# Optimization experiments

Hardware: AMD Instinct MI355X
Metric: run time of the kernel (lower is better)

## Reference

```python
import jax, jax.numpy as jnp
import numpy as np

N_E = 4096
E_DIM = 256
BETA = 0.25


def setup_inputs() -> dict:
    key = jax.random.key(0)
    k1, k2 = jax.random.split(key)
    z = jax.random.normal(k1, (2, E_DIM, 8, 32, 32), dtype=jnp.float32)
    # torch: embedding.weight.data.uniform_(-1/n_e, 1/n_e)
    embedding_weight = jax.random.uniform(
        k2, (N_E, E_DIM), dtype=jnp.float32, minval=-1.0 / N_E, maxval=1.0 / N_E)
    ema_embedding = jnp.zeros((N_E, E_DIM), dtype=jnp.float32)
    return {"z": z, "embedding_weight": embedding_weight, "ema_embedding": ema_embedding}


def reference(z, embedding_weight, ema_embedding):
    sg = jax.lax.stop_gradient
    # [B, C, D, H, W] -> [B, D, H, W, C]
    zp = jnp.transpose(z, (0, 2, 3, 4, 1))
    zf = zp.reshape(-1, E_DIM)  # [N, e_dim]
    # pairwise squared distances: ||z||^2 + ||e||^2 - 2 z e^T  -> [N, n_e]
    d = (jnp.sum(zf * zf, axis=1, keepdims=True)
         + jnp.sum(embedding_weight * embedding_weight, axis=1)
         - 2.0 * jnp.matmul(zf, embedding_weight.T))
    min_encoding_indices = jnp.argmin(d, axis=1)  # [N]
    min_encodings = jax.nn.one_hot(min_encoding_indices, N_E, dtype=zf.dtype)  # [N, n_e]
    # one_hot @ W == gather of codebook rows
    z_q = embedding_weight[min_encoding_indices].reshape(zp.shape)
    loss = (jnp.mean((sg(z_q) - zp) ** 2)
            + BETA * jnp.mean((z_q - sg(zp)) ** 2))
    # straight-through estimator
    z_q_st = zp + sg(z_q - zp)
    # EMA buffer update (torch does this under no_grad)
    ema_new = BETA * ema_embedding + (1.0 - BETA) * sg(embedding_weight)
    e_mean = jnp.mean(min_encodings, axis=0)
    perplexity = jnp.exp(-jnp.sum(e_mean * jnp.log(e_mean + 1e-10)))
    z_q_out = jnp.transpose(z_q_st, (0, 4, 1, 2, 3))
    z_out = jnp.transpose(zp, (0, 4, 1, 2, 3))
    return (loss, z_q_out, perplexity, min_encodings,
            min_encoding_indices[:, None], z_out, ema_new)
```

## Files before the change

kernel.cpp:

```cpp
#include <hip/hip_runtime.h>
#include <math.h>


#define N_E    4096
#define EDIM   256
#define SPAT   8192
#define NROWS  16384
#define ZELEMS 4194304
#define NCHUNK 32
#define NLOSSPARTS 16384

#define OFF_LOSS    0
#define OFF_ZQ      1
#define OFF_PERP    4194305
#define OFF_ONEHOT  4194306
#define OFF_IDX     71303170
#define OFF_ZOUT    71319554
#define OFF_EMA     75513858

#define SCR_WH_F   4
#define SCR_BD2_F  524292
#define SCR_ZH_F   71319556
#define SCR_WL_F   73416708
#define SCR_BD_F   73940996
#define SCR_BI_F   74465284

#define MARG 1.5e-4f
#define GAPM 1.5e-4f

typedef unsigned short u16;
typedef short short8 __attribute__((ext_vector_type(8)));
typedef float f32x4 __attribute__((ext_vector_type(4)));
typedef const void __attribute__((address_space(1)))* gas1;
typedef void __attribute__((address_space(3)))* las3;
#define GLOAD16(g, l) __builtin_amdgcn_global_load_lds((gas1)(g), (las3)(l), 16, 0, 0)

__device__ __forceinline__ u16 f2bf(float f) {
    unsigned u = __float_as_uint(f);
    return (u16)((u + 0x7fffu + ((u >> 16) & 1u)) >> 16);
}
__device__ __forceinline__ float bf2f(u16 h) {
    return __uint_as_float(((unsigned)h) << 16);
}

__global__ __launch_bounds__(256) void se_kernel(const float* __restrict__ W,
                                                 float* __restrict__ se) {
    int wid  = (blockIdx.x * 256 + threadIdx.x) >> 6;
    int lane = threadIdx.x & 63;
    if (wid < N_E) {
        const float4 v = *(const float4*)(W + (size_t)wid * EDIM + lane * 4);
        float s = v.x * v.x + v.y * v.y + v.z * v.z + v.w * v.w;
        #pragma unroll
        for (int off = 32; off > 0; off >>= 1) s += __shfl_down(s, off);
        if (lane == 0) se[wid] = s;
    }
}

__global__ __launch_bounds__(512) void rnorm_kernel(const float* __restrict__ z,
                                                    float* __restrict__ sz) {
    const int r0 = blockIdx.x * 128;
    const int bb = r0 >> 13;
    const int sp0 = r0 & (SPAT - 1);
    const float* zb = z + (size_t)bb * (EDIM * SPAT) + sp0;
    __shared__ float szp[4][128];
    const int lr = threadIdx.x & 127, kq = threadIdx.x >> 7;
    float s = 0.f;
    const float* p = zb + lr + (size_t)(kq * 64) * SPAT;
    for (int k = 0; k < 64; ++k) {
        float v = p[(size_t)k * SPAT];
        s += v * v;
    }
    szp[kq][lr] = s;
    __syncthreads();
    if (threadIdx.x < 128)
        sz[r0 + threadIdx.x] =
            ((szp[0][threadIdx.x] + szp[1][threadIdx.x]) + szp[2][threadIdx.x]) + szp[3][threadIdx.x];
}

__global__ __launch_bounds__(256) void split_w_kernel(const float* __restrict__ W,
                                                      u16* __restrict__ wh,
                                                      u16* __restrict__ wl) {
    const size_t t = (size_t)blockIdx.x * 256 + threadIdx.x;
    const float4 v = *(const float4*)(W + t * 4);
    u16 h0 = f2bf(v.x), h1 = f2bf(v.y), h2 = f2bf(v.z), h3 = f2bf(v.w);
    u16 l0 = f2bf(v.x - bf2f(h0)), l1 = f2bf(v.y - bf2f(h1));
    u16 l2 = f2bf(v.z - bf2f(h2)), l3 = f2bf(v.w - bf2f(h3));
    uint2 hp, lp;
    hp.x = (unsigned)h0 | ((unsigned)h1 << 16); hp.y = (unsigned)h2 | ((unsigned)h3 << 16);
    lp.x = (unsigned)l0 | ((unsigned)l1 << 16); lp.y = (unsigned)l2 | ((unsigned)l3 << 16);
    *(uint2*)(wh + t * 4) = hp;
    *(uint2*)(wl + t * 4) = lp;
}

__global__ __launch_bounds__(256) void split_z_kernel(const float* __restrict__ z,
                                                      u16* __restrict__ zh) {
    __shared__ float t[128][65];
    const int tid = threadIdx.x, wid = tid >> 6, lane = tid & 63;
    const int sp0 = blockIdx.x * 64, c0 = blockIdx.y * 128, b = blockIdx.z;
    const float* zb = z + (size_t)b * (EDIM * SPAT);
    #pragma unroll
    for (int it = 0; it < 32; ++it) {
        const int cl = wid + 4 * it;
        t[cl][lane] = zb[(size_t)(c0 + cl) * SPAT + sp0 + lane];
    }
    __syncthreads();
    #pragma unroll
    for (int it = 0; it < 16; ++it) {
        const int r = wid + 4 * it;
        const float v0 = t[2 * lane][r], v1 = t[2 * lane + 1][r];
        const u16 h0 = f2bf(v0), h1 = f2bf(v1);
        const size_t row = (size_t)b * SPAT + sp0 + r;
        ((unsigned*)zh)[row * 128 + (c0 >> 1) + lane] = (unsigned)h0 | ((unsigned)h1 << 16);
    }
}

__global__ __launch_bounds__(256, 3) void argmin_kernel(
        const u16* __restrict__ zh,
        const u16* __restrict__ wh, const u16* __restrict__ wl,
        const float* __restrict__ se, const float* __restrict__ sz,
        float* __restrict__ bD, int* __restrict__ bI,
        float* __restrict__ bD2, float* __restrict__ out_onehot) {
    __shared__ u16 sW[128][64];
    __shared__ u16 sZ[128][32];
    __shared__ float mD[2][128];
    __shared__ int   mI[2][128];
    __shared__ float mD2[2][128];

    const int tid = threadIdx.x;
    const int wid = tid >> 6, lane = tid & 63;
    const int wm = wid >> 1, wn = wid & 1;
    const int lq = lane >> 4, lr = lane & 15;
    const int chunk = blockIdx.x;
    const int rbase = blockIdx.y * 128;
    const int cbase = chunk * 128;

    const u16* gw[4];
    #pragma unroll
    for (int i = 0; i < 4; ++i) {
        const int o = i * 256 + tid;
        const int row = o >> 3, g = o & 7, u = g ^ (row & 7);
        const int ks = (u & 3) * 8;
        gw[i] = (u < 4 ? wh : wl) + (size_t)(cbase + row) * EDIM + ks;
    }
    const u16* gz[2];
    #pragma unroll
    for (int j = 0; j < 2; ++j) {
        const int o = j * 256 + tid;
        const int row = o >> 2, g = o & 3, u = g ^ ((row >> 1) & 3);
        gz[j] = zh + (size_t)(rbase + row) * EDIM + u * 8;
    }

    int aoff[4][2], boff[4];
    #pragma unroll
    for (int tt = 0; tt < 4; ++tt) {
        const int cl = wn * 64 + tt * 16 + lr;
        const int s0 = lq ^ (cl & 7);
        aoff[tt][0] = cl * 128 + s0 * 16;
        aoff[tt][1] = cl * 128 + (s0 ^ 4) * 16;
        const int rl = wm * 64 + tt * 16 + lr;
        boff[tt] = rl * 64 + (lq ^ ((rl >> 1) & 3)) * 16;
    }

    f32x4 acc[4][4];
    #pragma unroll
    for (int ci = 0; ci < 4; ++ci)
        #pragma unroll
        for (int rj = 0; rj < 4; ++rj) {
            f32x4 zzz = {0.f, 0.f, 0.f, 0.f};
            acc[ci][rj] = zzz;
        }

    const char* sWb = (const char*)&sW[0][0];
    const char* sZb = (const char*)&sZ[0][0];

    for (int k0 = 0; k0 < 8; ++k0) {
        __syncthreads();
        #pragma unroll
        for (int i = 0; i < 4; ++i) {
            GLOAD16(gw[i], (char*)&sW[0][0] + (i * 256 + wid * 64) * 16);
            gw[i] += 32;
        }
        #pragma unroll
        for (int j = 0; j < 2; ++j) {
            GLOAD16(gz[j], (char*)&sZ[0][0] + (j * 256 + wid * 64) * 16);
            gz[j] += 32;
        }
        __syncthreads();

        short8 zb[4];
        #pragma unroll
        for (int rj = 0; rj < 4; ++rj)
            zb[rj] = *(const short8*)(sZb + boff[rj]);
        #pragma unroll
        for (int ci = 0; ci < 4; ++ci) {
            const short8 wah = *(const short8*)(sWb + aoff[ci][0]);
            const short8 wal = *(const short8*)(sWb + aoff[ci][1]);
            #pragma unroll
            for (int rj = 0; rj < 4; ++rj) {
                acc[ci][rj] = __builtin_amdgcn_mfma_f32_16x16x32_bf16(wah, zb[rj], acc[ci][rj], 0, 0, 0);
                acc[ci][rj] = __builtin_amdgcn_mfma_f32_16x16x32_bf16(wal, zb[rj], acc[ci][rj], 0, 0, 0);
            }
        }
    }

    f32x4 sev[4];
    #pragma unroll
    for (int ci = 0; ci < 4; ++ci)
        sev[ci] = *(const f32x4*)(se + cbase + wn * 64 + ci * 16 + lq * 4);

    #pragma unroll
    for (int rj = 0; rj < 4; ++rj) {
        const int rloc = wm * 64 + rj * 16 + lr;
        const float szr = sz[rbase + rloc];
        float b1 = 3.4e38f, b2 = 3.4e38f; int bi1 = 0x7fffffff;
        #pragma unroll
        for (int ci = 0; ci < 4; ++ci) {
            #pragma unroll
            for (int r = 0; r < 4; ++r) {
                const float q = (szr + sev[ci][r]) - 2.0f * acc[ci][rj][r];
                const int code = cbase + wn * 64 + ci * 16 + lq * 4 + r;
                if (q < b1 || (q == b1 && code < bi1)) {
                    b2 = b1; b1 = q; bi1 = code;
                } else if (q < b2) {
                    b2 = q;
                }
            }
        }
        #pragma unroll
        for (int mask = 16; mask <= 32; mask <<= 1) {
            const float od1 = __shfl_xor(b1, mask);
            const int   oi1 = __shfl_xor(bi1, mask);
            const float od2 = __shfl_xor(b2, mask);
            const bool ot = (od1 < b1) || (od1 == b1 && oi1 < bi1);
            if (ot) { b2 = fminf(b1, od2); b1 = od1; bi1 = oi1; }
            else    { b2 = fminf(b2, od1); }
        }
        if (lq == 0) {
            mD[wn][rloc]  = b1;
            mI[wn][rloc]  = bi1;
            mD2[wn][rloc] = b2;
        }
    }
    __syncthreads();
    if (tid < 128) {
        const float d0 = mD[0][tid], d1 = mD[1][tid];
        const int   i0 = mI[0][tid], i1 = mI[1][tid];
        const float s0 = mD2[0][tid], s1 = mD2[1][tid];
        float dm, sm; int im;
        if (d1 < d0 || (d1 == d0 && i1 < i0)) { dm = d1; im = i1; sm = fminf(s1, d0); }
        else                                  { dm = d0; im = i0; sm = fminf(s0, d1); }
        bD [(size_t)chunk * NROWS + rbase + tid] = dm;
        bI [(size_t)chunk * NROWS + rbase + tid] = im;
        bD2[(size_t)chunk * NROWS + rbase + tid] = sm;
    }

    {
        const int slice = blockIdx.y * 32 + blockIdx.x;
        float* oh = out_onehot + (size_t)slice * 16384;
        const float4 z4 = {0.f, 0.f, 0.f, 0.f};
        #pragma unroll
        for (int it = 0; it < 16; ++it)
            *(float4*)(oh + it * 1024 + tid * 4) = z4;
    }
}

__global__ __launch_bounds__(256) void resolve_kernel(
        const float* __restrict__ z, const float* __restrict__ W,
        const float* __restrict__ se, const float* __restrict__ sz,
        const float* __restrict__ bD, const int* __restrict__ bI,
        const float* __restrict__ bD2,
        int* __restrict__ idx_ws, float* __restrict__ out_idx,
        float* __restrict__ out_onehot) {
    __shared__ float zr[EDIM];
    __shared__ float rd[128];
    __shared__ int   ri[128];
    __shared__ unsigned smask;
    __shared__ int swin, sskip;
    const int row = blockIdx.x;
    const int tid = threadIdx.x;

    if (tid < 64) {
        const int c = tid & 31;
        const float d1 = bD [(size_t)c * NROWS + row];
        const int   i1 = bI [(size_t)c * NROWS + row];
        const float d2 = bD2[(size_t)c * NROWS + row];
        float b1 = d1, b2 = d2; int j1 = i1;
        #pragma unroll
        for (int mask = 16; mask > 0; mask >>= 1) {
            const float od1 = __shfl_xor(b1, mask);
            const int   oj1 = __shfl_xor(j1, mask);
            const float od2 = __shfl_xor(b2, mask);
            const bool ot = (od1 < b1) || (od1 == b1 && oj1 < j1);
            if (ot) { b2 = fminf(b1, od2); b1 = od1; j1 = oj1; }
            else    { b2 = fminf(b2, od1); }
        }
        const unsigned long long m = __ballot(d1 <= b1 + MARG);
        if (tid == 0) {
            smask = (unsigned)(m & 0xffffffffu);
            swin  = j1;
            sskip = (b2 - b1 > GAPM) ? 1 : 0;
        }
    }
    __syncthreads();

    if (sskip) {
        if (tid == 0) {
            idx_ws[row]  = swin;
            out_idx[row] = (float)swin;
            out_onehot[(size_t)row * N_E + swin] = 1.0f;
        }
        return;
    }

    {
        const int b = row >> 13, sp = row & (SPAT - 1);
        zr[tid] = z[(size_t)b * (EDIM * SPAT) + (size_t)tid * SPAT + sp];
    }
    __syncthreads();

    const float szr = sz[row];
    unsigned cmask = smask;
    float best = 3.4e38f; int bi = 0x7fffffff;
    while (cmask) {
        const int cc = __ffs(cmask) - 1;
        cmask &= cmask - 1;
        if (tid < 128) {
            const int code = cc * 128 + tid;
            const float* wr = W + (size_t)code * EDIM;
            float s = 0.f;
            for (int k = 0; k < EDIM; ++k) s += zr[k] * wr[k];
            const float q = (szr + se[code]) - 2.0f * s;
            if (q < best || (q == best && code < bi)) { best = q; bi = code; }
        }
    }
    if (tid < 128) { rd[tid] = best; ri[tid] = bi; }
    __syncthreads();
    for (int off = 64; off > 0; off >>= 1) {
        if (tid < off) {
            const float od = rd[tid + off]; const int oi = ri[tid + off];
            if (od < rd[tid] || (od == rd[tid] && oi < ri[tid])) {
                rd[tid] = od; ri[tid] = oi;
            }
        }
        __syncthreads();
    }
    if (tid == 0) {
        const int ii = ri[0];
        idx_ws[row]  = ii;
        out_idx[row] = (float)ii;
        out_onehot[(size_t)row * N_E + ii] = 1.0f;
    }
}

__global__ __launch_bounds__(256) void outputs_kernel(
        const float* __restrict__ z, const float* __restrict__ W,
        const int* __restrict__ idx,
        float* __restrict__ zq_out, float* __restrict__ z_out,
        double* __restrict__ loss_parts) {
    const int t  = blockIdx.x * 256 + threadIdx.x;
    const float zv = z[t];
    const int sp = t & (SPAT - 1);
    const int c  = (t >> 13) & 255;
    const int b  = t >> 21;
    const int n  = (b << 13) + sp;
    const int id = idx[n];
    const float e    = W[id * EDIM + c];
    const float diff = e - zv;
    zq_out[t] = zv + diff;
    z_out[t]  = zv;

    double ds = (double)(diff * diff);
    #pragma unroll
    for (int off = 32; off > 0; off >>= 1) ds += __shfl_down(ds, off);
    __shared__ double bsum[4];
    const int lane = threadIdx.x & 63, w = threadIdx.x >> 6;
    if (lane == 0) bsum[w] = ds;
    __syncthreads();
    if (threadIdx.x == 0)
        loss_parts[blockIdx.x] = bsum[0] + bsum[1] + bsum[2] + bsum[3];
}

__global__ __launch_bounds__(256) void ema_kernel(const float* __restrict__ W,
                                                  const float* __restrict__ ema,
                                                  float* __restrict__ out) {
    const int t = blockIdx.x * 256 + threadIdx.x;
    out[t] = 0.25f * ema[t] + 0.75f * W[t];
}

__global__ __launch_bounds__(1024) void final_kernel(
        const int* __restrict__ idx, const double* __restrict__ loss_parts,
        float* __restrict__ out_loss, float* __restrict__ out_perp) {
    __shared__ int   hist[N_E];
    __shared__ float ps[1024];
    __shared__ double ls[1024];
    const int tid = threadIdx.x;

    for (int i = tid; i < N_E; i += 1024) hist[i] = 0;
    __syncthreads();
    for (int r = tid; r < NROWS; r += 1024) atomicAdd(&hist[idx[r]], 1);
    __syncthreads();

    float s = 0.f;
    for (int c = tid; c < N_E; c += 1024) {
        const float p = (float)hist[c] * (1.0f / (float)NROWS);
        s += p * logf(p + 1e-10f);
    }
    double l = 0.0;
    for (int c = tid; c < NLOSSPARTS; c += 1024) l += loss_parts[c];
    ps[tid] = s;
    ls[tid] = l;
    __syncthreads();
    for (int off = 512; off > 0; off >>= 1) {
        if (tid < off) {
            ps[tid] += ps[tid + off];
            ls[tid] += ls[tid + off];
        }
        __syncthreads();
    }
    if (tid == 0) {
        *out_perp = expf(-ps[0]);
        const float m = (float)(ls[0] / (double)ZELEMS);
        *out_loss = m + 0.25f * m;
    }
}

extern "C" void kernel_launch(void* const* d_in, const int* in_sizes, int n_in,
                              void* d_out, int out_size, void* d_ws, size_t ws_size,
                              hipStream_t stream) {
    const float* z   = (const float*)d_in[0];
    const float* W   = (const float*)d_in[1];
    const float* ema = (const float*)d_in[2];
    float* out = (float*)d_out;

    float* out_loss   = out + OFF_LOSS;
    float* out_zq     = out + OFF_ZQ;
    float* out_perp   = out + OFF_PERP;
    float* out_onehot = out + OFF_ONEHOT;
    float* out_idx    = out + OFF_IDX;
    float* out_z      = out + OFF_ZOUT;
    float* out_ema    = out + OFF_EMA;

    u16*   wh  = (u16*)(out + SCR_WH_F);
    float* bD2 = out + SCR_BD2_F;
    u16*   zh  = (u16*)(out + SCR_ZH_F);
    u16*   wl  = (u16*)(out + SCR_WL_F);
    float* bD  = out + SCR_BD_F;
    int*   bI  = (int*)(out + SCR_BI_F);

    char* ws = (char*)d_ws;
    float*  se    = (float*)ws;
    float*  sz    = (float*)(ws + 16384);
    int*    idxb  = (int*)  (ws + 81920);
    double* lossp = (double*)(ws + 147456);

    se_kernel<<<1024, 256, 0, stream>>>(W, se);
    rnorm_kernel<<<128, 512, 0, stream>>>(z, sz);
    split_w_kernel<<<1024, 256, 0, stream>>>(W, wh, wl);
    split_z_kernel<<<dim3(128, 2, 2), 256, 0, stream>>>(z, zh);
    argmin_kernel<<<dim3(NCHUNK, NROWS / 128), 256, 0, stream>>>(
        zh, wh, wl, se, sz, bD, bI, bD2, out_onehot);
    resolve_kernel<<<NROWS, 256, 0, stream>>>(z, W, se, sz, bD, bI, bD2,
                                              idxb, out_idx, out_onehot);
    outputs_kernel<<<ZELEMS / 256, 256, 0, stream>>>(z, W, idxb, out_zq, out_z,
                                                     lossp);
    ema_kernel<<<(N_E * EDIM) / 256, 256, 0, stream>>>(W, ema, out_ema);
    final_kernel<<<1, 1024, 0, stream>>>(idxb, lossp, out_loss, out_perp);
}
```

Baseline: 541.8 us.

## Double-buffer argmin LDS tiles and swap grid axes for codebook reuse

The argmin GEMM kernel now keeps two LDS buffers for the W and Z tiles and issues the global loads for the next K-step before computing on the current one, so there is one barrier per iteration instead of two. The grid is also transposed so that consecutive blocks share the same codebook chunk, which should improve L2 reuse of W. This doubles the LDS footprint to about 48KB per block, which may limit the intended occupancy of three blocks per CU.

```diff
diff --git a/kernel.cpp b/kernel.cpp
--- a/kernel.cpp
+++ b/kernel.cpp
@@ -120,8 +120,8 @@
         const float* __restrict__ se, const float* __restrict__ sz,
         float* __restrict__ bD, int* __restrict__ bI,
         float* __restrict__ bD2, float* __restrict__ out_onehot) {
-    __shared__ u16 sW[128][64];
-    __shared__ u16 sZ[128][32];
+    __shared__ u16 sW[2][128][64];
+    __shared__ u16 sZ[2][128][32];
     __shared__ float mD[2][128];
     __shared__ int   mI[2][128];
     __shared__ float mD2[2][128];
@@ -130,8 +130,8 @@
     const int wid = tid >> 6, lane = tid & 63;
     const int wm = wid >> 1, wn = wid & 1;
     const int lq = lane >> 4, lr = lane & 15;
-    const int chunk = blockIdx.x;
-    const int rbase = blockIdx.y * 128;
+    const int chunk = blockIdx.y;
+    const int rbase = blockIdx.x * 128;
     const int cbase = chunk * 128;
 
     const u16* gw[4];
@@ -149,6 +149,9 @@
         const int row = o >> 2, g = o & 3, u = g ^ ((row >> 1) & 3);
         gz[j] = zh + (size_t)(rbase + row) * EDIM + u * 8;
     }
+
+    char* sWb = (char*)&sW[0][0][0];
+    char* sZb = (char*)&sZ[0][0][0];
 
     int aoff[4][2], boff[4];
     #pragma unroll
@@ -170,38 +173,45 @@
             acc[ci][rj] = zzz;
         }
 
-    const char* sWb = (const char*)&sW[0][0];
-    const char* sZb = (const char*)&sZ[0][0];
+    #define STAGE(b) do {                                                      \
+        _Pragma("unroll")                                                      \
+        for (int i = 0; i < 4; ++i) {                                          \
+            GLOAD16(gw[i], sWb + (b) * 16384 + (i * 256 + wid * 64) * 16);     \
+            gw[i] += 32;                                                       \
+        }                                                                      \
+        _Pragma("unroll")                                                      \
+        for (int j = 0; j < 2; ++j) {                                          \
+            GLOAD16(gz[j], sZb + (b) * 8192 + (j * 256 + wid * 64) * 16);      \
+            gz[j] += 32;                                                       \
+        }                                                                      \
+    } while (0)
+
+    STAGE(0);
+    __syncthreads();
 
     for (int k0 = 0; k0 < 8; ++k0) {
-        __syncthreads();
-        #pragma unroll
-        for (int i = 0; i < 4; ++i) {
-            GLOAD16(gw[i], (char*)&sW[0][0] + (i * 256 + wid * 64) * 16);
-            gw[i] += 32;
-        }
-        #pragma unroll
-        for (int j = 0; j < 2; ++j) {
-            GLOAD16(gz[j], (char*)&sZ[0][0] + (j * 256 + wid * 64) * 16);
-            gz[j] += 32;
-        }
-        __syncthreads();
-
+        const int cur = k0 & 1;
+        if (k0 < 7) STAGE(cur ^ 1);
+
+        const char* wbase = sWb + cur * 16384;
+        const char* zbase = sZb + cur * 8192;
         short8 zb[4];
         #pragma unroll
         for (int rj = 0; rj < 4; ++rj)
-            zb[rj] = *(const short8*)(sZb + boff[rj]);
+            zb[rj] = *(const short8*)(zbase + boff[rj]);
         #pragma unroll
         for (int ci = 0; ci < 4; ++ci) {
-            const short8 wah = *(const short8*)(sWb + aoff[ci][0]);
-            const short8 wal = *(const short8*)(sWb + aoff[ci][1]);
+            const short8 wah = *(const short8*)(wbase + aoff[ci][0]);
+            const short8 wal = *(const short8*)(wbase + aoff[ci][1]);
             #pragma unroll
             for (int rj = 0; rj < 4; ++rj) {
                 acc[ci][rj] = __builtin_amdgcn_mfma_f32_16x16x32_bf16(wah, zb[rj], acc[ci][rj], 0, 0, 0);
                 acc[ci][rj] = __builtin_amdgcn_mfma_f32_16x16x32_bf16(wal, zb[rj], acc[ci][rj], 0, 0, 0);
             }
         }
-    }
+        __syncthreads();
+    }
+    #undef STAGE
 
     f32x4 sev[4];
     #pragma unroll
@@ -255,7 +265,7 @@
     }
 
     {
-        const int slice = blockIdx.y * 32 + blockIdx.x;
+        const int slice = blockIdx.x * 32 + blockIdx.y;
         float* oh = out_onehot + (size_t)slice * 16384;
         const float4 z4 = {0.f, 0.f, 0.f, 0.f};
         #pragma unroll
@@ -457,7 +467,7 @@
     rnorm_kernel<<<128, 512, 0, stream>>>(z, sz);
     split_w_kernel<<<1024, 256, 0, stream>>>(W, wh, wl);
     split_z_kernel<<<dim3(128, 2, 2), 256, 0, stream>>>(z, zh);
-    argmin_kernel<<<dim3(NCHUNK, NROWS / 128), 256, 0, stream>>>(
+    argmin_kernel<<<dim3(NROWS / 128, NCHUNK), 256, 0, stream>>>(
         zh, wh, wl, se, sz, bD, bI, bD2, out_onehot);
     resolve_kernel<<<NROWS, 256, 0, stream>>>(z, W, se, sz, bD, bI, bD2,
                                               idxb, out_idx, out_onehot);
```

New measurement: 550.2 us. About the same (+1.5%).
